# Performance work log

Measured on AMD Instinct MI355X. Metric: run time of the kernel, lower is better.

Reference implementation:

```python
import jax, jax.numpy as jnp
import numpy as np

DIM = 256
HEADS = 8
H = 56
W = 56
WS = 7          # window size
SHIFT = 3       # cyclic shift
MLP_HIDDEN = 4 * DIM
HEAD_DIM = DIM // HEADS
SCALE = HEAD_DIM ** -0.5
N = WS * WS     # tokens per window
EPS = 1e-5


def _rel_pos_index():
    coords = np.stack(np.meshgrid(np.arange(WS), np.arange(WS), indexing='ij'))  # [2,ws,ws]
    cf = coords.reshape(2, -1)                       # [2, N]
    rel = cf[:, :, None] - cf[:, None, :]            # [2, N, N]
    rel = rel.transpose(1, 2, 0).copy()              # [N, N, 2]
    rel[:, :, 0] += WS - 1
    rel[:, :, 1] += WS - 1
    rel[:, :, 1] *= 2 * WS - 1
    return rel.sum(-1)                               # [N, N]

REL_IDX = jnp.asarray(_rel_pos_index())


def _attn_mask():
    # shifted-window attention mask, computed once (static)
    img = np.zeros((H, W))
    cnt = 0
    slices = (slice(0, -WS), slice(-WS, -SHIFT), slice(-SHIFT, None))
    for hs in slices:
        for ws in slices:
            img[hs, ws] = cnt
            cnt += 1
    mw = img.reshape(H // WS, WS, W // WS, WS).transpose(0, 2, 1, 3).reshape(-1, N)  # [nW, N]
    am = mw[:, None, :] - mw[:, :, None]
    return jnp.asarray(np.where(am != 0, -100.0, 0.0).astype(np.float32))  # [nW, N, N]

ATTN_MASK = _attn_mask()


def _layernorm(y, g, b):
    mu = y.mean(-1, keepdims=True)
    var = ((y - mu) ** 2).mean(-1, keepdims=True)
    return (y - mu) * jax.lax.rsqrt(var + EPS) * g + b


def setup_inputs() -> dict:
    key = jax.random.key(0)
    ks = jax.random.split(key, 10)
    B = 32
    x = jax.random.normal(ks[0], (B, H * W, DIM), dtype=jnp.float32)
    qkv_w = jax.random.normal(ks[1], (DIM, 3 * DIM), dtype=jnp.float32) * 0.02
    qkv_b = jnp.zeros((3 * DIM,), dtype=jnp.float32)
    proj_w = jax.random.normal(ks[2], (DIM, DIM), dtype=jnp.float32) * 0.02
    proj_b = jnp.zeros((DIM,), dtype=jnp.float32)
    bias_table = jax.random.normal(ks[3], ((2 * WS - 1) * (2 * WS - 1), HEADS), dtype=jnp.float32) * 0.02
    norm1_g = jnp.ones((DIM,), dtype=jnp.float32)
    norm1_b = jnp.zeros((DIM,), dtype=jnp.float32)
    norm2_g = jnp.ones((DIM,), dtype=jnp.float32)
    norm2_b = jnp.zeros((DIM,), dtype=jnp.float32)
    mlp_w1 = jax.random.normal(ks[4], (DIM, MLP_HIDDEN), dtype=jnp.float32) * 0.02
    mlp_b1 = jnp.zeros((MLP_HIDDEN,), dtype=jnp.float32)
    mlp_w2 = jax.random.normal(ks[5], (MLP_HIDDEN, DIM), dtype=jnp.float32) * 0.02
    mlp_b2 = jnp.zeros((DIM,), dtype=jnp.float32)
    return dict(x=x, norm1_g=norm1_g, norm1_b=norm1_b, qkv_w=qkv_w, qkv_b=qkv_b,
                proj_w=proj_w, proj_b=proj_b, bias_table=bias_table,
                norm2_g=norm2_g, norm2_b=norm2_b,
                mlp_w1=mlp_w1, mlp_b1=mlp_b1, mlp_w2=mlp_w2, mlp_b2=mlp_b2)


def reference(x, norm1_g, norm1_b, qkv_w, qkv_b, proj_w, proj_b, bias_table,
              norm2_g, norm2_b, mlp_w1, mlp_b1, mlp_w2, mlp_b2):
    B, M, C = x.shape
    shortcut = x
    y = _layernorm(x, norm1_g, norm1_b).reshape(B, H, W, C)
    # cyclic shift
    y = jnp.roll(y, (-SHIFT, -SHIFT), axis=(1, 2))
    # window partition: [B,H,W,C] -> [B*nW, N, C]
    win = y.reshape(B, H // WS, WS, W // WS, WS, C).transpose(0, 1, 3, 2, 4, 5).reshape(-1, N, C)
    Bw = win.shape[0]
    qkv = (win @ qkv_w + qkv_b).reshape(Bw, N, 3, HEADS, HEAD_DIM).transpose(2, 0, 3, 1, 4)
    q, k, v = qkv[0], qkv[1], qkv[2]               # each [Bw, heads, N, hd]
    attn = jnp.einsum('bhnd,bhmd->bhnm', q, k) * SCALE
    bias = bias_table[REL_IDX].transpose(2, 0, 1)  # [heads, N, N]
    attn = attn + bias[None]
    nW = ATTN_MASK.shape[0]
    attn = attn.reshape(B, nW, HEADS, N, N) + ATTN_MASK[None, :, None]
    attn = jax.nn.softmax(attn.reshape(Bw, HEADS, N, N), axis=-1)
    out = jnp.einsum('bhnm,bhmd->bhnd', attn, v).transpose(0, 2, 1, 3).reshape(Bw, N, C)
    out = out @ proj_w + proj_b
    # window reverse and un-shift
    out = out.reshape(B, H // WS, W // WS, WS, WS, C).transpose(0, 1, 3, 2, 4, 5).reshape(B, H, W, C)
    out = jnp.roll(out, (SHIFT, SHIFT), axis=(1, 2)).reshape(B, M, C)
    x = shortcut + out
    h = _layernorm(x, norm2_g, norm2_b)
    h = jax.nn.gelu(h @ mlp_w1 + mlp_b1) @ mlp_w2 + mlp_b2
    return x + h
```

## Files before the change

kernel.cpp:

```cpp
#include <hip/hip_runtime.h>
#include <hip/hip_bf16.h>
#include <math.h>

typedef __bf16 bf16_t;
typedef __attribute__((ext_vector_type(8))) __bf16 bf16x8;
typedef __attribute__((ext_vector_type(4))) __bf16 bf16x4;
typedef __attribute__((ext_vector_type(4))) float f32x4;

#define T_TOK 100352
#define DIMC 256
#define HEADS 8
#define HD 32
#define NTOK 49
#define SHIFT3 3
#define HH 56
#define SCALE_QK 0.17677669529663687f

__device__ __forceinline__ int xrow_of(int rr) {
    int wi = rr / 49; int t = rr - wi * 49;
    int b = wi >> 6; int w64 = wi & 63;
    int wh = w64 >> 3, ww = w64 & 7;
    int i = t / 7, j = t - i * 7;
    int hy = wh * 7 + i, wy = ww * 7 + j;
    int hx = hy + SHIFT3; if (hx >= HH) hx -= HH;
    int wx = wy + SHIFT3; if (wx >= HH) wx -= HH;
    return b * (HH * HH) + hx * HH + wx;
}

__global__ __launch_bounds__(256) void transpose_cast(const float* __restrict__ W,
                                                      bf16_t* __restrict__ WT,
                                                      int K, int Nc) {
    int t = blockIdx.x * 256 + threadIdx.x;
    int k = t / Nc, c = t - k * Nc;
    WT[(size_t)c * K + k] = (bf16_t)W[t];
}

__global__ __launch_bounds__(256) void ln_kernel(const float* __restrict__ x,
                                                 const float* __restrict__ g,
                                                 const float* __restrict__ bsh,
                                                 bf16_t* __restrict__ out) {
    int wv = threadIdx.x >> 6, l = threadIdx.x & 63;
    int r = blockIdx.x * 4 + wv;
    int xr = xrow_of(r);
    float4 v = ((const float4*)(x + (size_t)xr * DIMC))[l];
    float s = v.x + v.y + v.z + v.w;
    float sq = v.x * v.x + v.y * v.y + v.z * v.z + v.w * v.w;
    #pragma unroll
    for (int off = 32; off; off >>= 1) {
        s += __shfl_down(s, off);
        sq += __shfl_down(sq, off);
    }
    s = __shfl(s, 0); sq = __shfl(sq, 0);
    float mean = s * (1.f / 256.f);
    float var = sq * (1.f / 256.f) - mean * mean;
    float rstd = rsqrtf(var + 1e-5f);
    float4 gv = ((const float4*)g)[l];
    float4 bv = ((const float4*)bsh)[l];
    bf16x4 o;
    o[0] = (bf16_t)((v.x - mean) * rstd * gv.x + bv.x);
    o[1] = (bf16_t)((v.y - mean) * rstd * gv.y + bv.y);
    o[2] = (bf16_t)((v.z - mean) * rstd * gv.z + bv.z);
    o[3] = (bf16_t)((v.w - mean) * rstd * gv.w + bv.w);
    *(bf16x4*)(out + (size_t)r * DIMC + l * 4) = o;
}

template <int EPI, int KT>
__global__ __launch_bounds__(256) void gemm128(const bf16_t* __restrict__ A,
                                               const bf16_t* __restrict__ BT,
                                               const float* __restrict__ bias,
                                               int Nc,
                                               bf16_t* __restrict__ outb,
                                               float* __restrict__ outf,
                                               const float* __restrict__ resid) {
    constexpr int NS = KT / 32;
    __shared__ bf16_t As[2][128 * 32];
    __shared__ bf16_t Bs[2][128 * 32];
    int tid = threadIdx.x;
    int wv = tid >> 6, l = tid & 63;
    int wr = wv >> 1, wc = wv & 1;
    int nTilesN = Nc >> 7;
    int qn = gridDim.x >> 3;
    int lb = (blockIdx.x & 7) * qn + (blockIdx.x >> 3);
    int bm = lb / nTilesN, bn = lb - bm * nTilesN;
    size_t row0 = (size_t)bm * 128;
    int col0 = bn * 128;

    const char* Abase = (const char*)(A + row0 * KT);
    const char* Bbase = (const char*)(BT + (size_t)col0 * KT);
    const size_t ldb = (size_t)KT * 2;

    auto STAGE = [&](int buf, int kk) {
        #pragma unroll
        for (int it = 0; it < 2; ++it) {
            int ci = tid + it * 256;
            int row = ci >> 2, ch = ci & 3;
            int sc = ch ^ (row & 3);
            __builtin_amdgcn_global_load_lds(
                (const __attribute__((address_space(1))) void*)(Abase + (size_t)row * ldb + (size_t)kk * 2 + sc * 16),
                (__attribute__((address_space(3))) void*)((char*)As[buf] + ci * 16), 16, 0, 0);
            __builtin_amdgcn_global_load_lds(
                (const __attribute__((address_space(1))) void*)(Bbase + (size_t)row * ldb + (size_t)kk * 2 + sc * 16),
                (__attribute__((address_space(3))) void*)((char*)Bs[buf] + ci * 16), 16, 0, 0);
        }
    };

    f32x4 acc[4][4] = {};
    const int lr = l & 15, g4 = l >> 4;

    STAGE(0, 0);

    for (int s = 0; s < NS; ++s) {
        int buf = s & 1;
        if (s + 1 < NS) {
            STAGE(buf ^ 1, (s + 1) * 32);
            asm volatile("s_waitcnt vmcnt(4)" ::: "memory");
        } else {
            asm volatile("s_waitcnt vmcnt(0)" ::: "memory");
        }
        __builtin_amdgcn_s_barrier();
        __builtin_amdgcn_sched_barrier(0);
        bf16x8 a[4], b[4];
        #pragma unroll
        for (int mt = 0; mt < 4; ++mt) {
            int rr = wr * 64 + mt * 16 + lr;
            int c = g4 ^ (rr & 3);
            a[mt] = *(const bf16x8*)((char*)As[buf] + rr * 64 + c * 16);
        }
        #pragma unroll
        for (int nt = 0; nt < 4; ++nt) {
            int rc = wc * 64 + nt * 16 + lr;
            int c = g4 ^ (rc & 3);
            b[nt] = *(const bf16x8*)((char*)Bs[buf] + rc * 64 + c * 16);
        }
        __builtin_amdgcn_s_setprio(1);
        #pragma unroll
        for (int mt = 0; mt < 4; ++mt)
            #pragma unroll
            for (int nt = 0; nt < 4; ++nt)
                acc[mt][nt] = __builtin_amdgcn_mfma_f32_16x16x32_bf16(a[mt], b[nt], acc[mt][nt], 0, 0, 0);
        __builtin_amdgcn_s_setprio(0);
        __builtin_amdgcn_sched_barrier(0);
        __builtin_amdgcn_s_barrier();
    }

    #pragma unroll
    for (int m = 0; m < 4; ++m) {
        #pragma unroll
        for (int i = 0; i < 4; ++i) {
            int rr = (int)row0 + wr * 64 + m * 16 + g4 * 4 + i;
            #pragma unroll
            for (int n = 0; n < 4; ++n) {
                int cc = col0 + wc * 64 + n * 16 + lr;
                float v = acc[m][n][i] + bias[cc];
                if (EPI == 0) {
                    outb[(size_t)rr * Nc + cc] = (bf16_t)v;
                } else if (EPI == 1) {
                    float t3 = v + 0.044715f * v * v * v;
                    float e = __expf(-1.5957691216057308f * t3);
                    float gl = v * __builtin_amdgcn_rcpf(1.f + e);
                    outb[(size_t)rr * Nc + cc] = (bf16_t)gl;
                } else {
                    size_t o = (size_t)rr * Nc + cc;
                    outf[o] = v + resid[o];
                }
            }
        }
    }
}

__global__ __launch_bounds__(256) void proj_ln(const bf16_t* __restrict__ A,
                                               const bf16_t* __restrict__ BT,
                                               const float* __restrict__ bias,
                                               const float* __restrict__ x,
                                               const float* __restrict__ g2,
                                               const float* __restrict__ b2,
                                               float* __restrict__ xmid,
                                               bf16_t* __restrict__ h2) {
    constexpr int NS = 8;
    __shared__ bf16_t As[2][64 * 32];
    __shared__ bf16_t Bs[2][256 * 32];
    int tid = threadIdx.x;
    int wv = tid >> 6, l = tid & 63;
    int lr = l & 15, g4 = l >> 4;
    int qn = gridDim.x >> 3;
    int lb = (blockIdx.x & 7) * qn + (blockIdx.x >> 3);
    size_t row0 = (size_t)lb * 64;

    const char* Abase = (const char*)(A + row0 * 256);
    const char* Bbase = (const char*)BT;

    auto STAGE = [&](int buf, int kk) {
        {
            int ci = tid;
            int row = ci >> 2, ch = ci & 3;
            int sc = ch ^ (row & 3);
            __builtin_amdgcn_global_load_lds(
                (const __attribute__((address_space(1))) void*)(Abase + (size_t)row * 512 + (size_t)kk * 2 + sc * 16),
                (__attribute__((address_space(3))) void*)((char*)As[buf] + ci * 16), 16, 0, 0);
        }
        #pragma unroll
        for (int it = 0; it < 4; ++it) {
            int ci = tid + it * 256;
            int row = ci >> 2, ch = ci & 3;
            int sc = ch ^ (row & 3);
            __builtin_amdgcn_global_load_lds(
                (const __attribute__((address_space(1))) void*)(Bbase + (size_t)row * 512 + (size_t)kk * 2 + sc * 16),
                (__attribute__((address_space(3))) void*)((char*)Bs[buf] + ci * 16), 16, 0, 0);
        }
    };

    f32x4 acc[16] = {};

    STAGE(0, 0);

    for (int s = 0; s < NS; ++s) {
        int buf = s & 1;
        if (s + 1 < NS) {
            STAGE(buf ^ 1, (s + 1) * 32);
            asm volatile("s_waitcnt vmcnt(5)" ::: "memory");
        } else {
            asm volatile("s_waitcnt vmcnt(0)" ::: "memory");
        }
        __builtin_amdgcn_s_barrier();
        __builtin_amdgcn_sched_barrier(0);
        bf16x8 a;
        {
            int rr = wv * 16 + lr;
            int c = g4 ^ (rr & 3);
            a = *(const bf16x8*)((char*)As[buf] + rr * 64 + c * 16);
        }
        bf16x8 b[16];
        #pragma unroll
        for (int nt = 0; nt < 16; ++nt) {
            int rc = nt * 16 + lr;
            int c = g4 ^ (rc & 3);
            b[nt] = *(const bf16x8*)((char*)Bs[buf] + rc * 64 + c * 16);
        }
        __builtin_amdgcn_s_setprio(1);
        #pragma unroll
        for (int nt = 0; nt < 16; ++nt)
            acc[nt] = __builtin_amdgcn_mfma_f32_16x16x32_bf16(a, b[nt], acc[nt], 0, 0, 0);
        __builtin_amdgcn_s_setprio(0);
        __builtin_amdgcn_sched_barrier(0);
        __builtin_amdgcn_s_barrier();
    }

    int xr[4];
    #pragma unroll
    for (int i = 0; i < 4; ++i) xr[i] = xrow_of((int)row0 + wv * 16 + g4 * 4 + i);

    float psum[4] = {0.f, 0.f, 0.f, 0.f}, psq[4] = {0.f, 0.f, 0.f, 0.f};
    #pragma unroll
    for (int n = 0; n < 16; ++n) {
        int cc = n * 16 + lr;
        float bv = bias[cc];
        #pragma unroll
        for (int i = 0; i < 4; ++i) {
            float v = acc[n][i] + bv + x[(size_t)xr[i] * 256 + cc];
            psum[i] += v; psq[i] += v * v;
        }
    }
    float mean[4], rstd[4];
    #pragma unroll
    for (int i = 0; i < 4; ++i) {
        float s = psum[i], q = psq[i];
        s += __shfl_xor(s, 1); q += __shfl_xor(q, 1);
        s += __shfl_xor(s, 2); q += __shfl_xor(q, 2);
        s += __shfl_xor(s, 4); q += __shfl_xor(q, 4);
        s += __shfl_xor(s, 8); q += __shfl_xor(q, 8);
        mean[i] = s * (1.f / 256.f);
        rstd[i] = rsqrtf(q * (1.f / 256.f) - mean[i] * mean[i] + 1e-5f);
    }
    #pragma unroll
    for (int n = 0; n < 16; ++n) {
        int cc = n * 16 + lr;
        float bv = bias[cc], gv = g2[cc], b2v = b2[cc];
        #pragma unroll
        for (int i = 0; i < 4; ++i) {
            size_t o = (size_t)xr[i] * 256 + cc;
            float v = acc[n][i] + bv + x[o];
            xmid[o] = v;
            h2[o] = (bf16_t)((v - mean[i]) * rstd[i] * gv + b2v);
        }
    }
}

__global__ __launch_bounds__(256) void attn_mfma(const bf16_t* __restrict__ qkv,
                                                 const float* __restrict__ bt,
                                                 bf16_t* __restrict__ out) {
    __shared__ __align__(16) char lds[4][12800];
    int wv = threadIdx.x >> 6, l = threadIdx.x & 63;
    int head = ((blockIdx.x & 1) << 2) | wv;
    int wi = blockIdx.x >> 1;
    char* W = lds[wv];
    bf16_t* Vt = (bf16_t*)(W + 8192);
    size_t rowbase = (size_t)wi * NTOK;
    const bf16_t* src = qkv + rowbase * 768 + head * HD;

    int w64 = wi & 63;
    int wh = w64 >> 3, ww = w64 & 7;
    bool lastH = (wh == 7), lastW = (ww == 7);
    bool masked = lastH || lastW;

    #pragma unroll
    for (int it = 0; it < 4; ++it) {
        int t = l + it * 64;
        int r = t >> 2, g = t & 3;
        if (r < NTOK) {
            bf16x8 qv = *(const bf16x8*)(src + (size_t)r * 768 + g * 8);
            bf16x8 kv = *(const bf16x8*)(src + (size_t)r * 768 + 256 + g * 8);
            int sa = (r * 64 + g * 16) ^ ((r & 7) << 4);
            *(bf16x8*)(W + sa) = qv;
            *(bf16x8*)(W + 4096 + sa) = kv;
        }
    }
    #pragma unroll
    for (int it = 0; it < 4; ++it) {
        int t = l + it * 64;
        int m = t >> 2, dc = t & 3;
        if (m < NTOK) {
            bf16x8 vv = *(const bf16x8*)(src + (size_t)m * 768 + 512 + dc * 8);
            #pragma unroll
            for (int j = 0; j < 8; ++j) Vt[(dc * 8 + j) * 72 + m] = vv[j];
        } else {
            #pragma unroll
            for (int j = 0; j < 8; ++j) Vt[(dc * 8 + j) * 72 + m] = (bf16_t)0.f;
        }
    }

    int lr = l & 15, g4 = l >> 4;

    bf16x8 a[4], b[4];
    #pragma unroll
    for (int mt = 0; mt < 4; ++mt) {
        int r = mt * 16 + lr;
        int sa = (r * 64 + g4 * 16) ^ ((r & 7) << 4);
        a[mt] = *(const bf16x8*)(W + sa);
        b[mt] = *(const bf16x8*)(W + 4096 + sa);
    }
    f32x4 z = {0.f, 0.f, 0.f, 0.f};
    f32x4 S[4][4];
    #pragma unroll
    for (int mt = 0; mt < 4; ++mt)
        #pragma unroll
        for (int nt = 0; nt < 4; ++nt)
            S[mt][nt] = __builtin_amdgcn_mfma_f32_16x16x32_bf16(a[mt], b[nt], z, 0, 0, 0);

    int i2[4], j2[4], reg2[4];
    #pragma unroll
    for (int nt = 0; nt < 4; ++nt) {
        int cm = nt * 16 + lr;
        i2[nt] = (cm * 147) >> 10;
        j2[nt] = cm - i2[nt] * 7;
        int rh = lastH ? ((i2[nt] < 4) ? 1 : 2) : 0;
        int rw = lastW ? ((j2[nt] < 4) ? 1 : 2) : 0;
        reg2[nt] = rh * 3 + rw;
    }

    #pragma unroll
    for (int mt = 0; mt < 4; ++mt) {
        #pragma unroll
        for (int i = 0; i < 4; ++i) {
            int rn = mt * 16 + g4 * 4 + i;
            bool rowok = rn < NTOK;
            int i1 = (rn * 147) >> 10, j1 = rn - i1 * 7;
            int rh1 = lastH ? ((i1 < 4) ? 1 : 2) : 0;
            int rw1 = lastW ? ((j1 < 4) ? 1 : 2) : 0;
            int reg1 = rh1 * 3 + rw1;
            float sv[4];
            #pragma unroll
            for (int nt = 0; nt < 4; ++nt) {
                int cm = nt * 16 + lr;
                float sc;
                if (rowok && cm < NTOK) {
                    sc = S[mt][nt][i] * SCALE_QK;
                    sc += bt[((i1 - i2[nt] + 6) + 13 * (j1 - j2[nt] + 6)) * 8 + head];
                    if (masked && (reg1 != reg2[nt])) sc -= 100.f;
                } else {
                    sc = -1e30f;
                }
                sv[nt] = sc;
            }
            float mx = fmaxf(fmaxf(sv[0], sv[1]), fmaxf(sv[2], sv[3]));
            mx = fmaxf(mx, __shfl_xor(mx, 1));
            mx = fmaxf(mx, __shfl_xor(mx, 2));
            mx = fmaxf(mx, __shfl_xor(mx, 4));
            mx = fmaxf(mx, __shfl_xor(mx, 8));
            float e[4];
            float sum = 0.f;
            #pragma unroll
            for (int nt = 0; nt < 4; ++nt) { e[nt] = __expf(sv[nt] - mx); sum += e[nt]; }
            sum += __shfl_xor(sum, 1);
            sum += __shfl_xor(sum, 2);
            sum += __shfl_xor(sum, 4);
            sum += __shfl_xor(sum, 8);
            float inv = 1.f / sum;
            #pragma unroll
            for (int nt = 0; nt < 4; ++nt) {
                int cm = nt * 16 + lr;
                int pa = (rn * 128 + cm * 2) ^ ((rn & 7) << 4);
                *(bf16_t*)(W + pa) = (bf16_t)(e[nt] * inv);
            }
        }
    }

    f32x4 o[4][2] = {};
    #pragma unroll
    for (int ks = 0; ks < 2; ++ks) {
        bf16x8 pa[4], vb[2];
        #pragma unroll
        for (int mt = 0; mt < 4; ++mt) {
            int r = mt * 16 + lr;
            int ad = (r * 128 + ks * 64 + g4 * 16) ^ ((r & 7) << 4);
            pa[mt] = *(const bf16x8*)(W + ad);
        }
        #pragma unroll
        for (int dt = 0; dt < 2; ++dt) {
            int d = dt * 16 + lr;
            vb[dt] = *(const bf16x8*)((char*)Vt + d * 144 + ks * 64 + g4 * 16);
        }
        #pragma unroll
        for (int mt = 0; mt < 4; ++mt)
            #pragma unroll
            for (int dt = 0; dt < 2; ++dt)
                o[mt][dt] = __builtin_amdgcn_mfma_f32_16x16x32_bf16(pa[mt], vb[dt], o[mt][dt], 0, 0, 0);
    }

    #pragma unroll
    for (int mt = 0; mt < 4; ++mt) {
        #pragma unroll
        for (int i = 0; i < 4; ++i) {
            int n = mt * 16 + g4 * 4 + i;
            if (n < NTOK) {
                #pragma unroll
                for (int dt = 0; dt < 2; ++dt) {
                    out[(rowbase + n) * DIMC + head * HD + dt * 16 + lr] = (bf16_t)o[mt][dt][i];
                }
            }
        }
    }
}

extern "C" void kernel_launch(void* const* d_in, const int* in_sizes, int n_in,
                              void* d_out, int out_size, void* d_ws, size_t ws_size,
                              hipStream_t stream) {
    const float* x      = (const float*)d_in[0];
    const float* n1g    = (const float*)d_in[1];
    const float* n1b    = (const float*)d_in[2];
    const float* qkv_w  = (const float*)d_in[3];
    const float* qkv_b  = (const float*)d_in[4];
    const float* proj_w = (const float*)d_in[5];
    const float* proj_b = (const float*)d_in[6];
    const float* btab   = (const float*)d_in[7];
    const float* n2g    = (const float*)d_in[8];
    const float* n2b    = (const float*)d_in[9];
    const float* w1     = (const float*)d_in[10];
    const float* b1     = (const float*)d_in[11];
    const float* w2     = (const float*)d_in[12];
    const float* b2     = (const float*)d_in[13];

    char* ws = (char*)d_ws;
    bf16_t* win      = (bf16_t*)(ws);
    bf16_t* qkvbuf   = (bf16_t*)(ws + (size_t)T_TOK * 256 * 2);
    bf16_t* mlp1_buf = (bf16_t*)(ws);
    bf16_t* h2       = (bf16_t*)(ws + (size_t)T_TOK * 2048);
    char* wtp        = ws + (size_t)T_TOK * 2048 + (size_t)T_TOK * 512;
    bf16_t* wt_qkv   = (bf16_t*)wtp;
    bf16_t* wt_proj  = wt_qkv + 768 * 256;
    bf16_t* wt_mlp1  = wt_proj + 256 * 256;
    bf16_t* wt_mlp2  = wt_mlp1 + 1024 * 256;
    float* xmid      = (float*)d_out;

    transpose_cast<<<768, 256, 0, stream>>>(qkv_w, wt_qkv, 256, 768);
    transpose_cast<<<256, 256, 0, stream>>>(proj_w, wt_proj, 256, 256);
    transpose_cast<<<1024, 256, 0, stream>>>(w1, wt_mlp1, 256, 1024);
    transpose_cast<<<1024, 256, 0, stream>>>(w2, wt_mlp2, 1024, 256);

    ln_kernel<<<T_TOK / 4, 256, 0, stream>>>(x, n1g, n1b, win);
    gemm128<0, 256><<<(T_TOK / 128) * (768 / 128), 256, 0, stream>>>(win, wt_qkv, qkv_b, 768,
                                                                     qkvbuf, nullptr, nullptr);
    attn_mfma<<<2048 * 2, 256, 0, stream>>>(qkvbuf, btab, win);
    proj_ln<<<T_TOK / 64, 256, 0, stream>>>(win, wt_proj, proj_b, x, n2g, n2b, xmid, h2);
    gemm128<1, 256><<<(T_TOK / 128) * (1024 / 128), 256, 0, stream>>>(h2, wt_mlp1, b1, 1024,
                                                                      mlp1_buf, nullptr, nullptr);
    gemm128<2, 1024><<<(T_TOK / 128) * (256 / 128), 256, 0, stream>>>(mlp1_buf, wt_mlp2, b2, 256,
                                                                      nullptr, xmid, xmid);
}
```

Baseline: 617.3 us.

## Double K-tile depth to 64 and prefetch two stages ahead in GEMMs

Both the generic 128x128 GEMM and the projection+LayerNorm GEMM now stage 64-wide K slices, with an 8-chunk XOR swizzle, instead of 32-wide ones. Loads are issued two stages ahead into the buffer that was just consumed, so each barrier covers twice the MFMA work. The aim is to halve the number of barriers and waits per K and keep more global loads in flight. In exchange, LDS use doubles per block, which may cut occupancy, and the hand-written vmcnt counts must match the new load counts.

```diff
diff --git a/kernel.cpp b/kernel.cpp
--- a/kernel.cpp
+++ b/kernel.cpp
@@ -72,9 +72,9 @@
                                                bf16_t* __restrict__ outb,
                                                float* __restrict__ outf,
                                                const float* __restrict__ resid) {
-    constexpr int NS = KT / 32;
-    __shared__ bf16_t As[2][128 * 32];
-    __shared__ bf16_t Bs[2][128 * 32];
+    constexpr int NS = KT / 64;
+    __shared__ bf16_t As[2][128 * 64];
+    __shared__ bf16_t Bs[2][128 * 64];
     int tid = threadIdx.x;
     int wv = tid >> 6, l = tid & 63;
     int wr = wv >> 1, wc = wv & 1;
@@ -91,10 +91,10 @@
 
     auto STAGE = [&](int buf, int kk) {
         #pragma unroll
-        for (int it = 0; it < 2; ++it) {
+        for (int it = 0; it < 4; ++it) {
             int ci = tid + it * 256;
-            int row = ci >> 2, ch = ci & 3;
-            int sc = ch ^ (row & 3);
+            int row = ci >> 3, ch = ci & 7;
+            int sc = ch ^ (row & 7);
             __builtin_amdgcn_global_load_lds(
                 (const __attribute__((address_space(1))) void*)(Abase + (size_t)row * ldb + (size_t)kk * 2 + sc * 16),
                 (__attribute__((address_space(3))) void*)((char*)As[buf] + ci * 16), 16, 0, 0);
@@ -108,39 +108,41 @@
     const int lr = l & 15, g4 = l >> 4;
 
     STAGE(0, 0);
-
+    if (NS > 1) STAGE(1, 64);
+
+    #pragma unroll
     for (int s = 0; s < NS; ++s) {
-        int buf = s & 1;
-        if (s + 1 < NS) {
-            STAGE(buf ^ 1, (s + 1) * 32);
-            asm volatile("s_waitcnt vmcnt(4)" ::: "memory");
-        } else {
-            asm volatile("s_waitcnt vmcnt(0)" ::: "memory");
-        }
+        if (s + 1 < NS) { asm volatile("s_waitcnt vmcnt(8)" ::: "memory"); }
+        else            { asm volatile("s_waitcnt vmcnt(0)" ::: "memory"); }
         __builtin_amdgcn_s_barrier();
         __builtin_amdgcn_sched_barrier(0);
-        bf16x8 a[4], b[4];
-        #pragma unroll
-        for (int mt = 0; mt < 4; ++mt) {
-            int rr = wr * 64 + mt * 16 + lr;
-            int c = g4 ^ (rr & 3);
-            a[mt] = *(const bf16x8*)((char*)As[buf] + rr * 64 + c * 16);
-        }
-        #pragma unroll
-        for (int nt = 0; nt < 4; ++nt) {
-            int rc = wc * 64 + nt * 16 + lr;
-            int c = g4 ^ (rc & 3);
-            b[nt] = *(const bf16x8*)((char*)Bs[buf] + rc * 64 + c * 16);
-        }
-        __builtin_amdgcn_s_setprio(1);
-        #pragma unroll
-        for (int mt = 0; mt < 4; ++mt)
-            #pragma unroll
-            for (int nt = 0; nt < 4; ++nt)
-                acc[mt][nt] = __builtin_amdgcn_mfma_f32_16x16x32_bf16(a[mt], b[nt], acc[mt][nt], 0, 0, 0);
-        __builtin_amdgcn_s_setprio(0);
+        int buf = s & 1;
+        #pragma unroll
+        for (int ks = 0; ks < 2; ++ks) {
+            bf16x8 a[4], b[4];
+            #pragma unroll
+            for (int mt = 0; mt < 4; ++mt) {
+                int rr = wr * 64 + mt * 16 + lr;
+                int c = (ks * 4 + g4) ^ (rr & 7);
+                a[mt] = *(const bf16x8*)((char*)As[buf] + rr * 128 + c * 16);
+            }
+            #pragma unroll
+            for (int nt = 0; nt < 4; ++nt) {
+                int rc = wc * 64 + nt * 16 + lr;
+                int c = (ks * 4 + g4) ^ (rc & 7);
+                b[nt] = *(const bf16x8*)((char*)Bs[buf] + rc * 128 + c * 16);
+            }
+            __builtin_amdgcn_s_setprio(1);
+            #pragma unroll
+            for (int mt = 0; mt < 4; ++mt)
+                #pragma unroll
+                for (int nt = 0; nt < 4; ++nt)
+                    acc[mt][nt] = __builtin_amdgcn_mfma_f32_16x16x32_bf16(a[mt], b[nt], acc[mt][nt], 0, 0, 0);
+            __builtin_amdgcn_s_setprio(0);
+        }
+        __builtin_amdgcn_s_barrier();
         __builtin_amdgcn_sched_barrier(0);
-        __builtin_amdgcn_s_barrier();
+        if (s + 2 < NS) STAGE(buf, (s + 2) * 64);
     }
 
     #pragma unroll
@@ -176,9 +178,9 @@
                                                const float* __restrict__ b2,
                                                float* __restrict__ xmid,
                                                bf16_t* __restrict__ h2) {
-    constexpr int NS = 8;
-    __shared__ bf16_t As[2][64 * 32];
-    __shared__ bf16_t Bs[2][256 * 32];
+    constexpr int NS = 4;
+    __shared__ bf16_t As[2][64 * 64];
+    __shared__ bf16_t Bs[2][256 * 64];
     int tid = threadIdx.x;
     int wv = tid >> 6, l = tid & 63;
     int lr = l & 15, g4 = l >> 4;
@@ -190,19 +192,20 @@
     const char* Bbase = (const char*)BT;
 
     auto STAGE = [&](int buf, int kk) {
-        {
-            int ci = tid;
-            int row = ci >> 2, ch = ci & 3;
-            int sc = ch ^ (row & 3);
+        #pragma unroll
+        for (int it = 0; it < 2; ++it) {
+            int ci = tid + it * 256;
+            int row = ci >> 3, ch = ci & 7;
+            int sc = ch ^ (row & 7);
             __builtin_amdgcn_global_load_lds(
                 (const __attribute__((address_space(1))) void*)(Abase + (size_t)row * 512 + (size_t)kk * 2 + sc * 16),
                 (__attribute__((address_space(3))) void*)((char*)As[buf] + ci * 16), 16, 0, 0);
         }
         #pragma unroll
-        for (int it = 0; it < 4; ++it) {
+        for (int it = 0; it < 8; ++it) {
             int ci = tid + it * 256;
-            int row = ci >> 2, ch = ci & 3;
-            int sc = ch ^ (row & 3);
+            int row = ci >> 3, ch = ci & 7;
+            int sc = ch ^ (row & 7);
             __builtin_amdgcn_global_load_lds(
                 (const __attribute__((address_space(1))) void*)(Bbase + (size_t)row * 512 + (size_t)kk * 2 + sc * 16),
                 (__attribute__((address_space(3))) void*)((char*)Bs[buf] + ci * 16), 16, 0, 0);
@@ -212,37 +215,39 @@
     f32x4 acc[16] = {};
 
     STAGE(0, 0);
-
+    STAGE(1, 64);
+
+    #pragma unroll
     for (int s = 0; s < NS; ++s) {
-        int buf = s & 1;
-        if (s + 1 < NS) {
-            STAGE(buf ^ 1, (s + 1) * 32);
-            asm volatile("s_waitcnt vmcnt(5)" ::: "memory");
-        } else {
-            asm volatile("s_waitcnt vmcnt(0)" ::: "memory");
-        }
+        if (s + 1 < NS) { asm volatile("s_waitcnt vmcnt(10)" ::: "memory"); }
+        else            { asm volatile("s_waitcnt vmcnt(0)" ::: "memory"); }
         __builtin_amdgcn_s_barrier();
         __builtin_amdgcn_sched_barrier(0);
-        bf16x8 a;
-        {
-            int rr = wv * 16 + lr;
-            int c = g4 ^ (rr & 3);
-            a = *(const bf16x8*)((char*)As[buf] + rr * 64 + c * 16);
-        }
-        bf16x8 b[16];
-        #pragma unroll
-        for (int nt = 0; nt < 16; ++nt) {
-            int rc = nt * 16 + lr;
-            int c = g4 ^ (rc & 3);
-            b[nt] = *(const bf16x8*)((char*)Bs[buf] + rc * 64 + c * 16);
-        }
-        __builtin_amdgcn_s_setprio(1);
-        #pragma unroll
-        for (int nt = 0; nt < 16; ++nt)
-            acc[nt] = __builtin_amdgcn_mfma_f32_16x16x32_bf16(a, b[nt], acc[nt], 0, 0, 0);
-        __builtin_amdgcn_s_setprio(0);
+        int buf = s & 1;
+        #pragma unroll
+        for (int ks = 0; ks < 2; ++ks) {
+            bf16x8 a;
+            {
+                int rr = wv * 16 + lr;
+                int c = (ks * 4 + g4) ^ (rr & 7);
+                a = *(const bf16x8*)((char*)As[buf] + rr * 128 + c * 16);
+            }
+            bf16x8 b[16];
+            #pragma unroll
+            for (int nt = 0; nt < 16; ++nt) {
+                int rc = nt * 16 + lr;
+                int c = (ks * 4 + g4) ^ (rc & 7);
+                b[nt] = *(const bf16x8*)((char*)Bs[buf] + rc * 128 + c * 16);
+            }
+            __builtin_amdgcn_s_setprio(1);
+            #pragma unroll
+            for (int nt = 0; nt < 16; ++nt)
+                acc[nt] = __builtin_amdgcn_mfma_f32_16x16x32_bf16(a, b[nt], acc[nt], 0, 0, 0);
+            __builtin_amdgcn_s_setprio(0);
+        }
+        __builtin_amdgcn_s_barrier();
         __builtin_amdgcn_sched_barrier(0);
-        __builtin_amdgcn_s_barrier();
+        if (s + 2 < NS) STAGE(buf, (s + 2) * 64);
     }
 
     int xr[4];
```

New measurement: 638.0 us. +3.4%, slower.
